# Kernel tuning notes

Measured on AMD Instinct MI355X. Metric: run time of the kernel, lower is better.

## Reference

```python
import jax, jax.numpy as jnp
import numpy as np

B, S, T = 32, 50, 50
V_SRC, V_TRG = 32000, 32000
E, H, A = 128, 128, 128


def setup_inputs() -> dict:
    key = jax.random.key(0)
    ks = jax.random.split(key, 24)
    g = lambda k, shape, s=0.08: jax.random.normal(k, shape, dtype=jnp.float32) * s
    inp = {
        'src': jax.random.randint(ks[0], (B, S), 0, V_SRC, dtype=jnp.int32),
        'trg': jax.random.randint(ks[1], (B, T), 0, V_TRG, dtype=jnp.int32),
        'emb_src': g(ks[2], (V_SRC, E)),
        'emb_trg': g(ks[3], (V_TRG, E)),
        # PyTorch LSTM params: gates ordered (i, f, g, o)
        'enc_Wih': g(ks[4], (4 * H, E)), 'enc_Whh': g(ks[5], (4 * H, H)),
        'enc_bih': g(ks[6], (4 * H,)), 'enc_bhh': g(ks[7], (4 * H,)),
        'dec_Wih': g(ks[8], (4 * H, E)), 'dec_Whh': g(ks[9], (4 * H, H)),
        'dec_bih': g(ks[10], (4 * H,)), 'dec_bhh': g(ks[11], (4 * H,)),
        'att_w1s': g(ks[12], (A, H)), 'att_b1s': g(ks[13], (A,)),
        'att_w1t': g(ks[14], (A, H)), 'att_b1t': g(ks[15], (A,)),
        'att_w2': g(ks[16], (1, A)), 'att_b2': g(ks[17], (1,)),
        'out_w': g(ks[18], (H, 2 * H)), 'out_b': g(ks[19], (H,)),
        'sm_w': g(ks[20], (V_TRG, H)), 'sm_b': g(ks[21], (V_TRG,)),
    }
    return inp


def _lstm_cell(x, h, c, Wih, Whh, bih, bhh):
    gates = x @ Wih.T + bih + h @ Whh.T + bhh  # [B, 4H]
    i, f, g, o = jnp.split(gates, 4, axis=-1)
    c_new = jax.nn.sigmoid(f) * c + jax.nn.sigmoid(i) * jnp.tanh(g)
    h_new = jax.nn.sigmoid(o) * jnp.tanh(c_new)
    return h_new, c_new


def reference(src, trg, emb_src, emb_trg,
              enc_Wih, enc_Whh, enc_bih, enc_bhh,
              dec_Wih, dec_Whh, dec_bih, dec_bhh,
              att_w1s, att_b1s, att_w1t, att_b1t, att_w2, att_b2,
              out_w, out_b, sm_w, sm_b):
    batch = src.shape[0]
    hidden = enc_Whh.shape[1]
    h0 = jnp.zeros((batch, hidden), dtype=emb_src.dtype)
    c0 = jnp.zeros((batch, hidden), dtype=emb_src.dtype)

    # ---- encoder LSTM over src ----
    x_src = emb_src[src]                      # [B,S,E]
    def enc_step(carry, x_t):
        h, c = carry
        h, c = _lstm_cell(x_t, h, c, enc_Wih, enc_Whh, enc_bih, enc_bhh)
        return (h, c), h
    _, enc_out = jax.lax.scan(enc_step, (h0, c0), x_src.transpose(1, 0, 2))
    enc_out = enc_out.transpose(1, 0, 2)      # [B,S,H]

    # att_w1_src(src_vectors) is constant across decode steps
    att_src = enc_out @ att_w1s.T + att_b1s   # [B,S,A]

    # ---- decoder (init_hidden = zeros, per original forward) ----
    x_trg = emb_trg[trg[:, :-1]]              # [B,T-1,E]
    def dec_step(carry, x_t):
        h, c = carry
        h, c = _lstm_cell(x_t, h, c, dec_Wih, dec_Whh, dec_bih, dec_bhh)
        att_tgt = h @ att_w1t.T + att_b1t                       # [B,A]
        comb = jnp.tanh(att_src + att_tgt[:, None, :])          # [B,S,A]
        scores = (comb @ att_w2.T + att_b2)[..., 0]             # [B,S]
        align = jax.nn.softmax(scores, axis=1)
        att_vec = jnp.einsum('bs,bsh->bh', align, enc_out)      # [B,H]
        final = jnp.tanh(jnp.concatenate([h, att_vec], axis=1) @ out_w.T + out_b)
        logits = final @ sm_w.T + sm_b                          # [B,V]
        return (h, c), logits
    _, logits = jax.lax.scan(dec_step, (h0, c0), x_trg.transpose(1, 0, 2))
    return logits.transpose(1, 0, 2)          # [B,T-1,V]
```

## Files before the change

### kernel.cpp

```cpp
#include <hip/hip_runtime.h>

typedef unsigned short ushort_t;
typedef __attribute__((ext_vector_type(2))) float f32x2;
typedef __attribute__((ext_vector_type(8))) short bfrag;
typedef __attribute__((ext_vector_type(4))) float f32x4;

__device__ __forceinline__ float sigf(float x) { return 1.0f / (1.0f + __expf(-x)); }
__device__ __forceinline__ float tanhf_fast(float x) { return 1.0f - 2.0f / (__expf(2.0f * x) + 1.0f); }
__device__ __forceinline__ ushort_t f2bf(float f) {
    unsigned u = __float_as_uint(f);
    unsigned r = (u + 0x7fffu + ((u >> 16) & 1u)) >> 16;
    return (ushort_t)r;
}

__global__ void prep_kernel(const float* __restrict__ eW, float* __restrict__ eWT,
                            const float* __restrict__ dW, float* __restrict__ dWT,
                            const float* __restrict__ w1s, float* __restrict__ w1sT,
                            const float* __restrict__ w1t, float* __restrict__ w1tT,
                            const float* __restrict__ ow, float* __restrict__ owT)
{
    int bid = blockIdx.x;
    int tid = threadIdx.x;
    __shared__ float tile[32][33];
    const float* in; float* outp; int C; int t;
    if (bid < 64)       { in = eW;  outp = eWT;  C = 128; t = bid; }
    else if (bid < 128) { in = dW;  outp = dWT;  C = 128; t = bid - 64; }
    else if (bid < 144) { in = w1s; outp = w1sT; C = 128; t = bid - 128; }
    else if (bid < 160) { in = w1t; outp = w1tT; C = 128; t = bid - 144; }
    else                { in = ow;  outp = owT;  C = 256; t = bid - 160; }
    int R = (bid < 128) ? 512 : 128;
    int gx = C >> 5;
    int c0 = (t & (gx - 1)) * 32, r0 = (t / gx) * 32;
    int x = tid & 31, y = tid >> 5;
#pragma unroll
    for (int i = 0; i < 32; i += 8)
        tile[y + i][x] = in[(r0 + y + i) * C + c0 + x];
    __syncthreads();
#pragma unroll
    for (int i = 0; i < 32; i += 8)
        outp[(c0 + y + i) * R + r0 + x] = tile[x][y + i];
}

__device__ __forceinline__ void tok_gemv_body(const float* __restrict__ X,
                                              const int* __restrict__ toks,
                                              int divv,
                                              const float* __restrict__ WT,
                                              const float* __restrict__ b1,
                                              const float* __restrict__ b2,
                                              float* __restrict__ out,
                                              int ntok, int n0, int J, float* xs)
{
    for (int i = threadIdx.x; i < 4 * 128; i += J) {
        int tt = i >> 7, k = i & 127;
        int n = n0 + tt;
        if (n >= ntok) n = ntok - 1;
        int row;
        if (!toks) row = n;
        else if (divv == 0) row = toks[n];
        else { int bb = n / divv; int t = n - bb * divv; row = toks[bb * (divv + 1) + t]; }
        xs[i] = X[row * 128 + k];
    }
    __syncthreads();
    int j = threadIdx.x;
    float bias = b1[j] + (b2 ? b2[j] : 0.0f);
    const float4* x0 = (const float4*)(xs);
    const float4* x1 = (const float4*)(xs + 128);
    const float4* x2 = (const float4*)(xs + 256);
    const float4* x3 = (const float4*)(xs + 384);
    float a0 = 0.f, a1 = 0.f, a2 = 0.f, a3 = 0.f;
#pragma unroll 8
    for (int k4 = 0; k4 < 32; ++k4) {
        float4 v0 = x0[k4], v1 = x1[k4], v2 = x2[k4], v3 = x3[k4];
        float w0 = WT[(k4 * 4 + 0) * J + j];
        float w1 = WT[(k4 * 4 + 1) * J + j];
        float w2_ = WT[(k4 * 4 + 2) * J + j];
        float w3 = WT[(k4 * 4 + 3) * J + j];
        a0 += v0.x * w0 + v0.y * w1 + v0.z * w2_ + v0.w * w3;
        a1 += v1.x * w0 + v1.y * w1 + v1.z * w2_ + v1.w * w3;
        a2 += v2.x * w0 + v2.y * w1 + v2.z * w2_ + v2.w * w3;
        a3 += v3.x * w0 + v3.y * w1 + v3.z * w2_ + v3.w * w3;
    }
    float accs[4] = {a0, a1, a2, a3};
#pragma unroll
    for (int tt = 0; tt < 4; ++tt) {
        int n = n0 + tt;
        if (n < ntok) out[n * J + j] = bias + accs[tt];
    }
}

__global__ void tok_gemv_kernel(const float* __restrict__ X,
                                const int* __restrict__ toks, int divv,
                                const float* __restrict__ WT,
                                const float* __restrict__ b1,
                                const float* __restrict__ b2,
                                float* __restrict__ out, int ntok)
{
    __shared__ __align__(16) float xs[4 * 128];
    tok_gemv_body(X, toks, divv, WT, b1, b2, out, ntok, blockIdx.x * 4, blockDim.x, xs);
}

__global__ void tok_gemv2_kernel(const float* __restrict__ embS, const int* __restrict__ src,
                                 const float* __restrict__ WTe,
                                 const float* __restrict__ bihE, const float* __restrict__ bhhE,
                                 float* __restrict__ gihE,
                                 const float* __restrict__ embT, const int* __restrict__ trg,
                                 const float* __restrict__ WTd,
                                 const float* __restrict__ bihD, const float* __restrict__ bhhD,
                                 float* __restrict__ gihD)
{
    __shared__ __align__(16) float xs[4 * 128];
    if (blockIdx.x < 400)
        tok_gemv_body(embS, src, 0, WTe, bihE, bhhE, gihE, 1600, blockIdx.x * 4, blockDim.x, xs);
    else
        tok_gemv_body(embT, trg, 49, WTd, bihD, bhhD, gihD, 1568, (blockIdx.x - 400) * 4, blockDim.x, xs);
}

__global__ void __launch_bounds__(512, 2) rnn_kernel(const float* __restrict__ gih_enc,
                                                     const float* __restrict__ enc_Whh,
                                                     const float* __restrict__ gih_dec,
                                                     const float* __restrict__ dec_Whh,
                                                     float* __restrict__ enc_out,
                                                     float* __restrict__ hdec)
{
    bool is_enc = blockIdx.x < 32;
    int b = is_enc ? blockIdx.x : blockIdx.x - 32;
    int T = is_enc ? 50 : 49;
    const float* gih = is_enc ? gih_enc : gih_dec;
    const float* Whh = is_enc ? enc_Whh : dec_Whh;
    float* hout = is_enc ? enc_out : hdec;

    int tid = threadIdx.x;
    __shared__ __align__(16) float h[128];
    __shared__ float gates[512];

    float4 w4[32];
    const float4* wr = (const float4*)(Whh + tid * 128);
#pragma unroll
    for (int k = 0; k < 32; ++k) w4[k] = wr[k];

    float c = 0.f;
    if (tid < 128) h[tid] = 0.f;
    const float* gb = gih + b * T * 512 + tid;
    float gnext = gb[0];
    const float4* h4 = (const float4*)h;
    int gt = tid >> 7;

    for (int t = 0; t < T; ++t) {
        __syncthreads();
        float g0 = gnext;
        if (t + 1 < T) gnext = gb[(t + 1) * 512];
        f32x2 s0 = {0.f, 0.f}, s1 = {0.f, 0.f};
#pragma unroll
        for (int k = 0; k < 32; ++k) {
            float4 hv = h4[k];
            f32x2 ha = {hv.x, hv.y}, hb = {hv.z, hv.w};
            f32x2 wa = {w4[k].x, w4[k].y}, wb = {w4[k].z, w4[k].w};
            s0 += ha * wa;
            s1 += hb * wb;
        }
        float acc = g0 + s0.x + s0.y + s1.x + s1.y;
        gates[tid] = (gt == 2) ? tanhf_fast(acc) : sigf(acc);
        __syncthreads();
        if (tid < 128) {
            float ai = gates[tid], af = gates[128 + tid], ag = gates[256 + tid], ao = gates[384 + tid];
            c = af * c + ai * ag;
            float hn = ao * tanhf_fast(c);
            h[tid] = hn;
            hout[(b * T + t) * 128 + tid] = hn;
        }
    }
}

__global__ void __launch_bounds__(128) att_par_kernel(const float* __restrict__ hdec,
                                                      const float* __restrict__ att_src,
                                                      const float* __restrict__ enc_out,
                                                      const float* __restrict__ w1tT,
                                                      const float* __restrict__ b1t,
                                                      const float* __restrict__ w2,
                                                      const float* __restrict__ b2,
                                                      const float* __restrict__ out_wT,
                                                      const float* __restrict__ out_b,
                                                      ushort_t* __restrict__ fin_bf)
{
    int b = blockIdx.y;
    int t0 = blockIdx.x * 2;
    int t1 = t0 + 1; if (t1 > 48) t1 = 48;
    int tid = threadIdx.x, lane = tid & 63, wv = tid >> 6;
    __shared__ __align__(16) float h0[128], h1[128];
    __shared__ __align__(16) float av0s[128], av1s[128];
    __shared__ float attt0[128], attt1[128];
    __shared__ float sc0[64], sc1[64];

    h0[tid] = hdec[(b * 49 + t0) * 128 + tid];
    h1[tid] = hdec[(b * 49 + t1) * 128 + tid];
    __syncthreads();
    const float4* h04 = (const float4*)h0;
    const float4* h14 = (const float4*)h1;

    {
        float acc0 = b1t[tid], acc1 = acc0;
#pragma unroll
        for (int k4 = 0; k4 < 32; ++k4) {
            float4 hv0 = h04[k4], hv1 = h14[k4];
            int k = k4 * 4;
            float wA = w1tT[(k + 0) * 128 + tid], wB = w1tT[(k + 1) * 128 + tid];
            float wC = w1tT[(k + 2) * 128 + tid], wD = w1tT[(k + 3) * 128 + tid];
            acc0 += hv0.x * wA + hv0.y * wB + hv0.z * wC + hv0.w * wD;
            acc1 += hv1.x * wA + hv1.y * wB + hv1.z * wC + hv1.w * wD;
        }
        attt0[tid] = acc0; attt1[tid] = acc1;
    }
    __syncthreads();
    {
        float w2a = w2[lane], w2b = w2[lane + 64], b2s = b2[0];
        float ta0 = attt0[lane], tb0 = attt0[lane + 64];
        float ta1 = attt1[lane], tb1 = attt1[lane + 64];
        const float* asb = att_src + b * 6400;
        for (int s = wv; s < 50; s += 2) {
            float lo = asb[s * 128 + lane], hi = asb[s * 128 + 64 + lane];
            float v0 = w2a * tanhf_fast(lo + ta0) + w2b * tanhf_fast(hi + tb0);
            float v1 = w2a * tanhf_fast(lo + ta1) + w2b * tanhf_fast(hi + tb1);
#pragma unroll
            for (int off = 32; off; off >>= 1) {
                v0 += __shfl_down(v0, off);
                v1 += __shfl_down(v1, off);
            }
            if (lane == 0) { sc0[s] = v0 + b2s; sc1[s] = v1 + b2s; }
        }
    }
    __syncthreads();
    {
        float* scp = wv ? sc1 : sc0;
        float x = (lane < 50) ? scp[lane] : -1e30f;
        float m = x;
#pragma unroll
        for (int off = 32; off; off >>= 1) m = fmaxf(m, __shfl_xor(m, off));
        float e = (lane < 50) ? __expf(x - m) : 0.f;
        float ssum = e;
#pragma unroll
        for (int off = 32; off; off >>= 1) ssum += __shfl_xor(ssum, off);
        if (lane < 50) scp[lane] = e / ssum;
    }
    __syncthreads();
    {
        const float* eob = enc_out + b * 6400;
        float a0 = 0.f, a1 = 0.f;
        for (int s = 0; s < 50; ++s) {
            float ev = eob[s * 128 + tid];
            a0 += sc0[s] * ev; a1 += sc1[s] * ev;
        }
        av0s[tid] = a0; av1s[tid] = a1;
    }
    __syncthreads();
    {
        const float4* a04 = (const float4*)av0s;
        const float4* a14 = (const float4*)av1s;
        float f0 = out_b[tid], f1 = f0;
#pragma unroll
        for (int k4 = 0; k4 < 32; ++k4) {
            float4 hv0 = h04[k4], hv1 = h14[k4];
            int k = k4 * 4;
            float wA = out_wT[(k + 0) * 128 + tid], wB = out_wT[(k + 1) * 128 + tid];
            float wC = out_wT[(k + 2) * 128 + tid], wD = out_wT[(k + 3) * 128 + tid];
            f0 += hv0.x * wA + hv0.y * wB + hv0.z * wC + hv0.w * wD;
            f1 += hv1.x * wA + hv1.y * wB + hv1.z * wC + hv1.w * wD;
        }
#pragma unroll
        for (int k4 = 0; k4 < 32; ++k4) {
            float4 v0 = a04[k4], v1 = a14[k4];
            int k = 128 + k4 * 4;
            float wA = out_wT[(k + 0) * 128 + tid], wB = out_wT[(k + 1) * 128 + tid];
            float wC = out_wT[(k + 2) * 128 + tid], wD = out_wT[(k + 3) * 128 + tid];
            f0 += v0.x * wA + v0.y * wB + v0.z * wC + v0.w * wD;
            f1 += v1.x * wA + v1.y * wB + v1.z * wC + v1.w * wD;
        }
        fin_bf[(b * 49 + t0) * 128 + tid] = f2bf(tanhf_fast(f0));
        fin_bf[(b * 49 + t1) * 128 + tid] = f2bf(tanhf_fast(f1));
    }
}

__global__ void __launch_bounds__(256) logits_gemm_kernel(const ushort_t* __restrict__ A,
                                                          const float* __restrict__ Bw,
                                                          const float* __restrict__ bias,
                                                          float* __restrict__ out)
{
    int wv = threadIdx.x >> 6, lane = threadIdx.x & 63;
    int r = lane & 15, kq = (lane >> 4) * 8;
    int nb = blockIdx.x * 64 + wv * 16;

    bfrag bf[4];
    {
        const float* bp = Bw + (size_t)(nb + r) * 128 + kq;
#pragma unroll
        for (int kk = 0; kk < 4; ++kk) {
            float4 lo = *(const float4*)(bp + kk * 32);
            float4 hi = *(const float4*)(bp + kk * 32 + 4);
            bfrag f;
            f[0] = (short)f2bf(lo.x); f[1] = (short)f2bf(lo.y);
            f[2] = (short)f2bf(lo.z); f[3] = (short)f2bf(lo.w);
            f[4] = (short)f2bf(hi.x); f[5] = (short)f2bf(hi.y);
            f[6] = (short)f2bf(hi.z); f[7] = (short)f2bf(hi.w);
            bf[kk] = f;
        }
    }
    int colq = (lane >> 4) * 4;
    float4 bs = *(const float4*)(bias + nb + colq);

    const ushort_t* ab = A + r * 128 + kq;
    bfrag a0 = *(const bfrag*)(ab);
    bfrag a1 = *(const bfrag*)(ab + 32);
    bfrag a2 = *(const bfrag*)(ab + 64);
    bfrag a3 = *(const bfrag*)(ab + 96);

    for (int mt = 0; mt < 98; ++mt) {
        bfrag c0 = a0, c1 = a1, c2 = a2, c3 = a3;
        if (mt < 97) {
            const ushort_t* np = ab + (mt + 1) * 16 * 128;
            a0 = *(const bfrag*)(np);
            a1 = *(const bfrag*)(np + 32);
            a2 = *(const bfrag*)(np + 64);
            a3 = *(const bfrag*)(np + 96);
        }
        f32x4 acc = {0.f, 0.f, 0.f, 0.f};
        acc = __builtin_amdgcn_mfma_f32_16x16x32_bf16(bf[0], c0, acc, 0, 0, 0);
        acc = __builtin_amdgcn_mfma_f32_16x16x32_bf16(bf[1], c1, acc, 0, 0, 0);
        acc = __builtin_amdgcn_mfma_f32_16x16x32_bf16(bf[2], c2, acc, 0, 0, 0);
        acc = __builtin_amdgcn_mfma_f32_16x16x32_bf16(bf[3], c3, acc, 0, 0, 0);
        int m = mt * 16 + r;
        float4 st = {acc[0] + bs.x, acc[1] + bs.y, acc[2] + bs.z, acc[3] + bs.w};
        *(float4*)(out + (size_t)m * 32000 + nb + colq) = st;
    }
}

extern "C" void kernel_launch(void* const* d_in, const int* in_sizes, int n_in,
                              void* d_out, int out_size, void* d_ws, size_t ws_size,
                              hipStream_t stream)
{
    const int* src      = (const int*)d_in[0];
    const int* trg      = (const int*)d_in[1];
    const float* emb_src = (const float*)d_in[2];
    const float* emb_trg = (const float*)d_in[3];
    const float* enc_Wih = (const float*)d_in[4];
    const float* enc_Whh = (const float*)d_in[5];
    const float* enc_bih = (const float*)d_in[6];
    const float* enc_bhh = (const float*)d_in[7];
    const float* dec_Wih = (const float*)d_in[8];
    const float* dec_Whh = (const float*)d_in[9];
    const float* dec_bih = (const float*)d_in[10];
    const float* dec_bhh = (const float*)d_in[11];
    const float* att_w1s = (const float*)d_in[12];
    const float* att_b1s = (const float*)d_in[13];
    const float* att_w1t = (const float*)d_in[14];
    const float* att_b1t = (const float*)d_in[15];
    const float* att_w2  = (const float*)d_in[16];
    const float* att_b2  = (const float*)d_in[17];
    const float* out_w   = (const float*)d_in[18];
    const float* out_b   = (const float*)d_in[19];
    const float* sm_w    = (const float*)d_in[20];
    const float* sm_b    = (const float*)d_in[21];
    float* out = (float*)d_out;

    char* ws = (char*)d_ws;
    float*    gih_enc = (float*)(ws);
    float*    att_src = (float*)(ws);
    float*    gih_dec = (float*)(ws + 3276800);
    ushort_t* fin_bf  = (ushort_t*)(ws + 3276800);
    float*    enc_out = (float*)(ws + 6488064);
    float*    hdec    = (float*)(ws + 7307264);
    float*    WihT_e  = (float*)(ws + 8110080);
    float*    WihT_d  = (float*)(ws + 8372224);
    float*    w1sT    = (float*)(ws + 8634368);
    float*    w1tT    = (float*)(ws + 8699904);
    float*    outwT   = (float*)(ws + 8765440);

    prep_kernel<<<192, 256, 0, stream>>>(enc_Wih, WihT_e, dec_Wih, WihT_d,
                                         att_w1s, w1sT, att_w1t, w1tT,
                                         out_w, outwT);

    tok_gemv2_kernel<<<792, 512, 0, stream>>>(emb_src, src, WihT_e, enc_bih, enc_bhh, gih_enc,
                                              emb_trg, trg, WihT_d, dec_bih, dec_bhh, gih_dec);

    rnn_kernel<<<64, 512, 0, stream>>>(gih_enc, enc_Whh, gih_dec, dec_Whh, enc_out, hdec);

    tok_gemv_kernel<<<400, 128, 0, stream>>>(enc_out, nullptr, 0, w1sT, att_b1s, nullptr, att_src, 1600);

    att_par_kernel<<<dim3(25, 32), 128, 0, stream>>>(hdec, att_src, enc_out,
                                                     w1tT, att_b1t, att_w2, att_b2,
                                                     outwT, out_b, fin_bf);

    logits_gemm_kernel<<<500, 256, 0, stream>>>(fin_bf, sm_w, sm_b, out);
}
```

Measured before the change: 438.7 us.

## Fuse att_src projection into encoder RNN and widen token GEMV tiles

The att_w1s projection of encoder outputs moves into the encoder recurrence. Each encoder block keeps a slice of att_w1s in registers and computes the projection of the previous step's h alongside the gate math, which removes a separate kernel launch and its transpose. The token-embedding GEMV now handles 8 tokens per block instead of 4, so each loaded weight is reused more often. Logits output stores become nontemporal. The trade-off is extra register pressure in rnn_kernel, since launch_bounds no longer requests 2 blocks per CU, and more work on the latency-critical serial path.

```diff
diff --git a/kernel.cpp b/kernel.cpp
--- a/kernel.cpp
+++ b/kernel.cpp
@@ -15,7 +15,6 @@
 
 __global__ void prep_kernel(const float* __restrict__ eW, float* __restrict__ eWT,
                             const float* __restrict__ dW, float* __restrict__ dWT,
-                            const float* __restrict__ w1s, float* __restrict__ w1sT,
                             const float* __restrict__ w1t, float* __restrict__ w1tT,
                             const float* __restrict__ ow, float* __restrict__ owT)
 {
@@ -25,9 +24,8 @@
     const float* in; float* outp; int C; int t;
     if (bid < 64)       { in = eW;  outp = eWT;  C = 128; t = bid; }
     else if (bid < 128) { in = dW;  outp = dWT;  C = 128; t = bid - 64; }
-    else if (bid < 144) { in = w1s; outp = w1sT; C = 128; t = bid - 128; }
-    else if (bid < 160) { in = w1t; outp = w1tT; C = 128; t = bid - 144; }
-    else                { in = ow;  outp = owT;  C = 256; t = bid - 160; }
+    else if (bid < 144) { in = w1t; outp = w1tT; C = 128; t = bid - 128; }
+    else                { in = ow;  outp = owT;  C = 256; t = bid - 144; }
     int R = (bid < 128) ? 512 : 128;
     int gx = C >> 5;
     int c0 = (t & (gx - 1)) * 32, r0 = (t / gx) * 32;
@@ -41,86 +39,68 @@
         outp[(c0 + y + i) * R + r0 + x] = tile[x][y + i];
 }
 
-__device__ __forceinline__ void tok_gemv_body(const float* __restrict__ X,
-                                              const int* __restrict__ toks,
-                                              int divv,
-                                              const float* __restrict__ WT,
-                                              const float* __restrict__ b1,
-                                              const float* __restrict__ b2,
-                                              float* __restrict__ out,
-                                              int ntok, int n0, int J, float* xs)
-{
-    for (int i = threadIdx.x; i < 4 * 128; i += J) {
+__global__ void __launch_bounds__(512) tok_gemv2_kernel(
+    const float* __restrict__ embS, const int* __restrict__ src,
+    const float* __restrict__ WTe,
+    const float* __restrict__ bihE, const float* __restrict__ bhhE,
+    float* __restrict__ gihE,
+    const float* __restrict__ embT, const int* __restrict__ trg,
+    const float* __restrict__ WTd,
+    const float* __restrict__ bihD, const float* __restrict__ bhhD,
+    float* __restrict__ gihD)
+{
+    __shared__ __align__(16) float xs[8 * 128];
+    const float* X; const int* toks; int divv; const float* WT;
+    const float* b1; const float* b2; float* out; int ntok; int n0;
+    if (blockIdx.x < 200) {
+        X = embS; toks = src; divv = 0;  WT = WTe; b1 = bihE; b2 = bhhE;
+        out = gihE; ntok = 1600; n0 = blockIdx.x * 8;
+    } else {
+        X = embT; toks = trg; divv = 49; WT = WTd; b1 = bihD; b2 = bhhD;
+        out = gihD; ntok = 1568; n0 = (blockIdx.x - 200) * 8;
+    }
+    int tid = threadIdx.x;
+    for (int i = tid; i < 8 * 128; i += 512) {
         int tt = i >> 7, k = i & 127;
         int n = n0 + tt;
         if (n >= ntok) n = ntok - 1;
         int row;
-        if (!toks) row = n;
-        else if (divv == 0) row = toks[n];
+        if (divv == 0) row = toks[n];
         else { int bb = n / divv; int t = n - bb * divv; row = toks[bb * (divv + 1) + t]; }
         xs[i] = X[row * 128 + k];
     }
     __syncthreads();
-    int j = threadIdx.x;
-    float bias = b1[j] + (b2 ? b2[j] : 0.0f);
-    const float4* x0 = (const float4*)(xs);
-    const float4* x1 = (const float4*)(xs + 128);
-    const float4* x2 = (const float4*)(xs + 256);
-    const float4* x3 = (const float4*)(xs + 384);
-    float a0 = 0.f, a1 = 0.f, a2 = 0.f, a3 = 0.f;
-#pragma unroll 8
+    int j = tid;
+    float bias = b1[j] + b2[j];
+    float acc[8] = {0.f, 0.f, 0.f, 0.f, 0.f, 0.f, 0.f, 0.f};
+#pragma unroll 4
     for (int k4 = 0; k4 < 32; ++k4) {
-        float4 v0 = x0[k4], v1 = x1[k4], v2 = x2[k4], v3 = x3[k4];
-        float w0 = WT[(k4 * 4 + 0) * J + j];
-        float w1 = WT[(k4 * 4 + 1) * J + j];
-        float w2_ = WT[(k4 * 4 + 2) * J + j];
-        float w3 = WT[(k4 * 4 + 3) * J + j];
-        a0 += v0.x * w0 + v0.y * w1 + v0.z * w2_ + v0.w * w3;
-        a1 += v1.x * w0 + v1.y * w1 + v1.z * w2_ + v1.w * w3;
-        a2 += v2.x * w0 + v2.y * w1 + v2.z * w2_ + v2.w * w3;
-        a3 += v3.x * w0 + v3.y * w1 + v3.z * w2_ + v3.w * w3;
-    }
-    float accs[4] = {a0, a1, a2, a3};
-#pragma unroll
-    for (int tt = 0; tt < 4; ++tt) {
+        float w0 = WT[(k4 * 4 + 0) * 512 + j];
+        float w1 = WT[(k4 * 4 + 1) * 512 + j];
+        float w2_ = WT[(k4 * 4 + 2) * 512 + j];
+        float w3 = WT[(k4 * 4 + 3) * 512 + j];
+#pragma unroll
+        for (int tt = 0; tt < 8; ++tt) {
+            float4 v = ((const float4*)(xs + tt * 128))[k4];
+            acc[tt] += v.x * w0 + v.y * w1 + v.z * w2_ + v.w * w3;
+        }
+    }
+#pragma unroll
+    for (int tt = 0; tt < 8; ++tt) {
         int n = n0 + tt;
-        if (n < ntok) out[n * J + j] = bias + accs[tt];
-    }
-}
-
-__global__ void tok_gemv_kernel(const float* __restrict__ X,
-                                const int* __restrict__ toks, int divv,
-                                const float* __restrict__ WT,
-                                const float* __restrict__ b1,
-                                const float* __restrict__ b2,
-                                float* __restrict__ out, int ntok)
-{
-    __shared__ __align__(16) float xs[4 * 128];
-    tok_gemv_body(X, toks, divv, WT, b1, b2, out, ntok, blockIdx.x * 4, blockDim.x, xs);
-}
-
-__global__ void tok_gemv2_kernel(const float* __restrict__ embS, const int* __restrict__ src,
-                                 const float* __restrict__ WTe,
-                                 const float* __restrict__ bihE, const float* __restrict__ bhhE,
-                                 float* __restrict__ gihE,
-                                 const float* __restrict__ embT, const int* __restrict__ trg,
-                                 const float* __restrict__ WTd,
-                                 const float* __restrict__ bihD, const float* __restrict__ bhhD,
-                                 float* __restrict__ gihD)
-{
-    __shared__ __align__(16) float xs[4 * 128];
-    if (blockIdx.x < 400)
-        tok_gemv_body(embS, src, 0, WTe, bihE, bhhE, gihE, 1600, blockIdx.x * 4, blockDim.x, xs);
-    else
-        tok_gemv_body(embT, trg, 49, WTd, bihD, bhhD, gihD, 1568, (blockIdx.x - 400) * 4, blockDim.x, xs);
-}
-
-__global__ void __launch_bounds__(512, 2) rnn_kernel(const float* __restrict__ gih_enc,
-                                                     const float* __restrict__ enc_Whh,
-                                                     const float* __restrict__ gih_dec,
-                                                     const float* __restrict__ dec_Whh,
-                                                     float* __restrict__ enc_out,
-                                                     float* __restrict__ hdec)
+        if (n < ntok) out[n * 512 + j] = bias + acc[tt];
+    }
+}
+
+__global__ void __launch_bounds__(512) rnn_kernel(const float* __restrict__ gih_enc,
+                                                  const float* __restrict__ enc_Whh,
+                                                  const float* __restrict__ gih_dec,
+                                                  const float* __restrict__ dec_Whh,
+                                                  const float* __restrict__ w1s,
+                                                  const float* __restrict__ b1s,
+                                                  float* __restrict__ enc_out,
+                                                  float* __restrict__ hdec,
+                                                  float* __restrict__ att_src)
 {
     bool is_enc = blockIdx.x < 32;
     int b = is_enc ? blockIdx.x : blockIdx.x - 32;
@@ -130,13 +110,25 @@
     float* hout = is_enc ? enc_out : hdec;
 
     int tid = threadIdx.x;
+    int j = tid & 127, part = tid >> 7;
     __shared__ __align__(16) float h[128];
     __shared__ float gates[512];
+    __shared__ float asum[512];
 
     float4 w4[32];
     const float4* wr = (const float4*)(Whh + tid * 128);
 #pragma unroll
     for (int k = 0; k < 32; ++k) w4[k] = wr[k];
+
+    float4 ws4[8];
+    float b1sr = 0.f;
+    if (is_enc) {
+        const float4* wsr = (const float4*)(w1s + j * 128 + part * 32);
+#pragma unroll
+        for (int k = 0; k < 8; ++k) ws4[k] = wsr[k];
+        if (tid < 128) b1sr = b1s[tid];
+    }
+    float* asb = att_src + b * 6400;
 
     float c = 0.f;
     if (tid < 128) h[tid] = 0.f;
@@ -160,6 +152,17 @@
         }
         float acc = g0 + s0.x + s0.y + s1.x + s1.y;
         gates[tid] = (gt == 2) ? tanhf_fast(acc) : sigf(acc);
+        if (is_enc && t > 0) {
+            f32x2 p0 = {0.f, 0.f}, p1 = {0.f, 0.f};
+#pragma unroll
+            for (int k = 0; k < 8; ++k) {
+                float4 hv = h4[part * 8 + k];
+                f32x2 ha = {hv.x, hv.y}, hb = {hv.z, hv.w};
+                f32x2 wa = {ws4[k].x, ws4[k].y}, wb = {ws4[k].z, ws4[k].w};
+                p0 += ha * wa; p1 += hb * wb;
+            }
+            asum[tid] = p0.x + p0.y + p1.x + p1.y;
+        }
         __syncthreads();
         if (tid < 128) {
             float ai = gates[tid], af = gates[128 + tid], ag = gates[256 + tid], ao = gates[384 + tid];
@@ -167,7 +170,26 @@
             float hn = ao * tanhf_fast(c);
             h[tid] = hn;
             hout[(b * T + t) * 128 + tid] = hn;
-        }
+            if (is_enc && t > 0)
+                asb[(t - 1) * 128 + tid] = b1sr + asum[tid] + asum[128 + tid]
+                                         + asum[256 + tid] + asum[384 + tid];
+        }
+    }
+    if (is_enc) {
+        __syncthreads();
+        f32x2 p0 = {0.f, 0.f}, p1 = {0.f, 0.f};
+#pragma unroll
+        for (int k = 0; k < 8; ++k) {
+            float4 hv = h4[part * 8 + k];
+            f32x2 ha = {hv.x, hv.y}, hb = {hv.z, hv.w};
+            f32x2 wa = {ws4[k].x, ws4[k].y}, wb = {ws4[k].z, ws4[k].w};
+            p0 += ha * wa; p1 += hb * wb;
+        }
+        asum[tid] = p0.x + p0.y + p1.x + p1.y;
+        __syncthreads();
+        if (tid < 128)
+            asb[49 * 128 + tid] = b1sr + asum[tid] + asum[128 + tid]
+                                + asum[256 + tid] + asum[384 + tid];
     }
 }
 
@@ -327,8 +349,8 @@
         acc = __builtin_amdgcn_mfma_f32_16x16x32_bf16(bf[2], c2, acc, 0, 0, 0);
         acc = __builtin_amdgcn_mfma_f32_16x16x32_bf16(bf[3], c3, acc, 0, 0, 0);
         int m = mt * 16 + r;
-        float4 st = {acc[0] + bs.x, acc[1] + bs.y, acc[2] + bs.z, acc[3] + bs.w};
-        *(float4*)(out + (size_t)m * 32000 + nb + colq) = st;
+        f32x4 st = {acc[0] + bs.x, acc[1] + bs.y, acc[2] + bs.z, acc[3] + bs.w};
+        __builtin_nontemporal_store(st, (f32x4*)(out + (size_t)m * 32000 + nb + colq));
     }
 }
 
@@ -362,27 +384,24 @@
 
     char* ws = (char*)d_ws;
     float*    gih_enc = (float*)(ws);
-    float*    att_src = (float*)(ws);
     float*    gih_dec = (float*)(ws + 3276800);
     ushort_t* fin_bf  = (ushort_t*)(ws + 3276800);
     float*    enc_out = (float*)(ws + 6488064);
     float*    hdec    = (float*)(ws + 7307264);
-    float*    WihT_e  = (float*)(ws + 8110080);
-    float*    WihT_d  = (float*)(ws + 8372224);
-    float*    w1sT    = (float*)(ws + 8634368);
-    float*    w1tT    = (float*)(ws + 8699904);
-    float*    outwT   = (float*)(ws + 8765440);
-
-    prep_kernel<<<192, 256, 0, stream>>>(enc_Wih, WihT_e, dec_Wih, WihT_d,
-                                         att_w1s, w1sT, att_w1t, w1tT,
-                                         out_w, outwT);
-
-    tok_gemv2_kernel<<<792, 512, 0, stream>>>(emb_src, src, WihT_e, enc_bih, enc_bhh, gih_enc,
+    float*    att_src = (float*)(ws + 8110080);
+    float*    w1tT    = (float*)(ws + 8929280);
+    float*    outwT   = (float*)(ws + 8994816);
+    float*    WihT_e  = (float*)(ws + 9125888);
+    float*    WihT_d  = (float*)(ws + 9388032);
+
+    prep_kernel<<<176, 256, 0, stream>>>(enc_Wih, WihT_e, dec_Wih, WihT_d,
+                                         att_w1t, w1tT, out_w, outwT);
+
+    tok_gemv2_kernel<<<396, 512, 0, stream>>>(emb_src, src, WihT_e, enc_bih, enc_bhh, gih_enc,
                                               emb_trg, trg, WihT_d, dec_bih, dec_bhh, gih_dec);
 
-    rnn_kernel<<<64, 512, 0, stream>>>(gih_enc, enc_Whh, gih_dec, dec_Whh, enc_out, hdec);
-
-    tok_gemv_kernel<<<400, 128, 0, stream>>>(enc_out, nullptr, 0, w1sT, att_b1s, nullptr, att_src, 1600);
+    rnn_kernel<<<64, 512, 0, stream>>>(gih_enc, enc_Whh, gih_dec, dec_Whh,
+                                       att_w1s, att_b1s, enc_out, hdec, att_src);
 
     att_par_kernel<<<dim3(25, 32), 128, 0, stream>>>(hdec, att_src, enc_out,
                                                      w1tT, att_b1t, att_w2, att_b2,
```

New measurement: 446.7 us. No clear change (+1.8%).
